# Performance work log

Measured on AMD Instinct MI355X. Metric: run time of the kernel, lower is better.

The kernel has to match this reference:

```python
import jax, jax.numpy as jnp
import numpy as np

B, H, S, D = 2, 16, 8192, 128
NUM_REFLECTIONS = D // 2
ROPE_BASE = 10000.0


def setup_inputs() -> dict:
    key = jax.random.key(0)
    kq, kk, kv = jax.random.split(key, 3)
    q = jax.random.normal(kq, (B, H, S, D), dtype=jnp.float32)
    k = jax.random.normal(kk, (B, H, S, D), dtype=jnp.float32)
    vs = jax.random.normal(kv, (NUM_REFLECTIONS, D), dtype=jnp.float32) * 0.02
    # standard RoPE cos/sin buffer, rotate-half layout: angles duplicated over both halves
    inv_freq = 1.0 / (ROPE_BASE ** (jnp.arange(0, D, 2, dtype=jnp.float32) / D))  # [D/2]
    ang = jnp.arange(S, dtype=jnp.float32)[:, None] * inv_freq[None, :]           # [S, D/2]
    emb = jnp.concatenate([ang, ang], axis=-1)                                    # [S, D]
    cos = jnp.broadcast_to(jnp.cos(emb)[None], (B, S, D))
    sin = jnp.broadcast_to(jnp.sin(emb)[None], (B, S, D))
    return {"q": q, "k": k, "vs": vs, "cos": cos, "sin": sin}


def _householder_matrix(vs):
    # Q = prod of Householder reflections applied left-to-right, as in get_matrix()
    eye = jnp.eye(vs.shape[-1], dtype=vs.dtype)
    def step(Q, v):
        v_norm_sq = jnp.sum(v * v) + 1e-8
        Q = Q - (2.0 / v_norm_sq) * jnp.outer(v, v @ Q)
        return Q, None
    Q, _ = jax.lax.scan(step, eye, vs)
    return Q


def _rotate_half(x):
    d2 = x.shape[-1] // 2
    return jnp.concatenate([-x[..., d2:], x[..., :d2]], axis=-1)


def reference(q, k, vs, cos, sin):
    Q = _householder_matrix(vs)                 # [D, D]
    # inverse transform: x @ Q.T
    qi = jnp.einsum("bhsd,ed->bhse", q, Q)
    ki = jnp.einsum("bhsd,ed->bhse", k, Q)
    c = cos[:, None, :, :]                      # [B,1,S,D] broadcast over heads
    s = sin[:, None, :, :]
    q_rot = qi * c + _rotate_half(qi) * s
    k_rot = ki * c + _rotate_half(ki) * s
    # forward transform: x @ Q
    q_final = jnp.einsum("bhsd,de->bhse", q_rot, Q)
    k_final = jnp.einsum("bhsd,de->bhse", k_rot, Q)
    return (q_final, k_final)
```

## Files before the change

### kernel.cpp

```cpp
#include <hip/hip_runtime.h>

typedef __bf16 bf16x8 __attribute__((ext_vector_type(8)));
typedef __bf16 bf16x4 __attribute__((ext_vector_type(4)));
typedef __bf16 bf16x2 __attribute__((ext_vector_type(2)));
typedef float  f32x4  __attribute__((ext_vector_type(4)));
typedef int    i32x4  __attribute__((ext_vector_type(4)));

static constexpr int kS = 8192;
static constexpr int kD = 128;
static constexpr int kRowsPerTensor = 2 * 16 * kS;
static constexpr int kFragElems = kD * kD;

__global__ __launch_bounds__(1024) void rnrope_build_q(
    const float* __restrict__ vs,
    __bf16* __restrict__ wsQA,
    __bf16* __restrict__ wsQf) {
  __shared__ float vsh[64 * 128];
  const int tid = threadIdx.x;
  for (int i = tid; i < 2048; i += 1024)
    ((float4*)vsh)[i] = ((const float4*)vs)[i];
  __syncthreads();

  const int col  = blockIdx.x * 16 + (tid >> 6);
  const int lane = tid & 63;

  float qlo = (col == lane)      ? 1.0f : 0.0f;
  float qhi = (col == lane + 64) ? 1.0f : 0.0f;

  for (int r = 0; r < 64; ++r) {
    float vlo = vsh[r * 128 + lane];
    float vhi = vsh[r * 128 + lane + 64];
    float t0 = vlo * qlo + vhi * qhi;
    float t1 = vlo * vlo + vhi * vhi;
    #pragma unroll
    for (int off = 32; off > 0; off >>= 1) {
      t0 += __shfl_xor(t0, off);
      t1 += __shfl_xor(t1, off);
    }
    float sf = 2.0f / (t1 + 1e-8f) * t0;
    qlo -= sf * vlo;
    qhi -= sf * vhi;
  }

  {
    const int ks = col >> 5, qdc = (col >> 3) & 3, jj = col & 7;
    #pragma unroll
    for (int h = 0; h < 2; ++h) {
      int i = lane + h * 64;
      float val = h ? qhi : qlo;
      int mt = i >> 4, rl = i & 15;
      wsQA[((mt * 4 + ks) * 64 + qdc * 16 + rl) * 8 + jj] = (__bf16)val;
    }
  }
  {
    const int nt = col >> 4;
    const int nn = col & 15;
    #pragma unroll
    for (int h = 0; h < 2; ++h) {
      int i = lane + h * 64;
      float val = h ? qhi : qlo;
      int ks = i >> 5, qdc = (i >> 3) & 3, jj = i & 7;
      wsQf[((ks * 8 + nt) * 64 + qdc * 16 + nn) * 8 + jj] = (__bf16)val;
    }
  }
}

__global__ __launch_bounds__(512, 4) void rnrope_main(
    const float* __restrict__ qg, const float* __restrict__ kg,
    const __bf16* __restrict__ wsQA, const __bf16* __restrict__ wsQf,
    float* __restrict__ outg) {
  __shared__ __align__(16) __bf16 lds[2 * kFragElems];
  __bf16* ldsQ = lds;
  __bf16* ldsX = lds + kFragElems;

  const int tid    = threadIdx.x;
  const int blk    = blockIdx.x;
  const int tensor = blk >> 11;
  const int tile   = blk & 2047;
  const float* __restrict__ Xg = tensor ? kg : qg;
  float* __restrict__ Og = outg + (size_t)tensor * (size_t)kRowsPerTensor * kD;
  const int row0 = tile * 128;

  #pragma unroll
  for (int i = 0; i < 4; ++i)
    ((uint4*)ldsQ)[tid + i * 512] = ((const uint4*)wsQA)[tid + i * 512];

  #pragma unroll
  for (int it = 0; it < 8; ++it) {
    int f    = tid + it * 512;
    int mloc = f >> 5;
    int q4   = f & 31;
    int k0   = q4 * 4;
    float4 x4 = ((const float4*)(Xg + (size_t)(row0 + mloc) * kD))[q4];
    int ks = k0 >> 5, qdc = (k0 >> 3) & 3, j = k0 & 7;
    int w = mloc >> 4, m = mloc & 15;
    int idx = ((w * 4 + ks) * 64 + qdc * 16 + m) * 8 + j;
    bf16x4 v;
    v[0] = (__bf16)x4.x; v[1] = (__bf16)x4.y; v[2] = (__bf16)x4.z; v[3] = (__bf16)x4.w;
    *(bf16x4*)(&ldsX[idx]) = v;
  }
  __syncthreads();

  const int w    = tid >> 6;
  const int lane = tid & 63;
  const int qd   = lane >> 4;
  const int cc   = lane & 15;

  bf16x8 xb[4];
  #pragma unroll
  for (int ks = 0; ks < 4; ++ks)
    xb[ks] = *(const bf16x8*)(&ldsX[((w * 4 + ks) * 64 + lane) * 8]);

  f32x4 acc[8];
  #pragma unroll
  for (int mt = 0; mt < 8; ++mt) acc[mt] = (f32x4){0.f, 0.f, 0.f, 0.f};
  #pragma unroll
  for (int mt = 0; mt < 8; ++mt) {
    #pragma unroll
    for (int ks = 0; ks < 4; ++ks) {
      bf16x8 a1 = *(const bf16x8*)(&ldsQ[((mt * 4 + ks) * 64 + lane) * 8]);
      acc[mt] = __builtin_amdgcn_mfma_f32_16x16x32_bf16(a1, xb[ks], acc[mt], 0, 0, 0);
    }
  }

  const float kNegL = -0.20762050593046967f;
  {
    float spos = (float)((row0 + w * 16 + cc) & (kS - 1));
    #pragma unroll
    for (int mt = 0; mt < 4; ++mt) {
      #pragma unroll
      for (int reg = 0; reg < 4; ++reg) {
        float fe  = (float)(mt * 16 + qd * 4 + reg);
        float ang = spos * exp2f(kNegL * fe);
        float sv, cv;
        __sincosf(ang, &sv, &cv);
        float ylo = acc[mt][reg];
        float yhi = acc[mt + 4][reg];
        acc[mt][reg]     = ylo * cv - yhi * sv;
        acc[mt + 4][reg] = yhi * cv + ylo * sv;
      }
    }
  }

  int pw[16];
  #pragma unroll
  for (int mt = 0; mt < 8; ++mt) {
    #pragma unroll
    for (int p = 0; p < 2; ++p) {
      bf16x2 t;
      t[0] = (__bf16)acc[mt][2 * p];
      t[1] = (__bf16)acc[mt][2 * p + 1];
      pw[mt * 2 + p] = __builtin_bit_cast(int, t);
    }
  }
  bf16x8 a2[4];
  #pragma unroll
  for (int ks = 0; ks < 4; ++ks) {
    i32x4 aw;
    #pragma unroll
    for (int jw = 0; jw < 4; ++jw) {
      int srcl = ((((2 * qd + (jw >> 1)) & 3) * 16) + cc) * 4;
      int wlo = __builtin_amdgcn_ds_bpermute(srcl, pw[4 * ks + (jw & 1)]);
      int whi = __builtin_amdgcn_ds_bpermute(srcl, pw[4 * ks + 2 + (jw & 1)]);
      aw[jw] = (qd < 2) ? wlo : whi;
    }
    a2[ks] = __builtin_bit_cast(bf16x8, aw);
  }

  #pragma unroll
  for (int nt = 0; nt < 8; ++nt) acc[nt] = (f32x4){0.f, 0.f, 0.f, 0.f};
  #pragma unroll
  for (int nt = 0; nt < 8; ++nt) {
    #pragma unroll
    for (int ks = 0; ks < 4; ++ks) {
      bf16x8 b2 = *(const bf16x8*)(wsQf + ((ks * 8 + nt) * 64 + lane) * 8);
      acc[nt] = __builtin_amdgcn_mfma_f32_16x16x32_bf16(a2[ks], b2, acc[nt], 0, 0, 0);
    }
  }

  float* __restrict__ Ob = Og + (size_t)(row0 + w * 16) * kD;
  #pragma unroll
  for (int nt = 0; nt < 8; ++nt) {
    #pragma unroll
    for (int reg = 0; reg < 4; ++reg)
      Ob[(qd * 4 + reg) * kD + nt * 16 + cc] = acc[nt][reg];
  }
}

extern "C" void kernel_launch(void* const* d_in, const int* in_sizes, int n_in,
                              void* d_out, int out_size, void* d_ws, size_t ws_size,
                              hipStream_t stream) {
  const float* q  = (const float*)d_in[0];
  const float* k  = (const float*)d_in[1];
  const float* vs = (const float*)d_in[2];
  __bf16* wsQA = (__bf16*)d_ws;
  __bf16* wsQf = wsQA + kFragElems;

  rnrope_build_q<<<8, 1024, 0, stream>>>(vs, wsQA, wsQf);
  rnrope_main<<<4096, 512, 0, stream>>>(q, k, wsQA, wsQf, (float*)d_out);
}
```

Baseline: 492.6 us.

## Make main kernel persistent over 64-row tiles with register prefetch of next tile

```diff
diff --git a/kernel.cpp b/kernel.cpp
--- a/kernel.cpp
+++ b/kernel.cpp
@@ -10,6 +10,9 @@
 static constexpr int kD = 128;
 static constexpr int kRowsPerTensor = 2 * 16 * kS;
 static constexpr int kFragElems = kD * kD;
+static constexpr int kTileRows = 64;
+static constexpr int kTilesPerBlock = 8;
+static constexpr int kTilesPerTensor = kRowsPerTensor / kTileRows;
 
 __global__ __launch_bounds__(1024) void rnrope_build_q(
     const float* __restrict__ vs,
@@ -65,125 +68,159 @@
   }
 }
 
-__global__ __launch_bounds__(512, 4) void rnrope_main(
+__device__ __forceinline__ void lds_barrier() {
+  asm volatile("s_waitcnt lgkmcnt(0)" ::: "memory");
+  __builtin_amdgcn_s_barrier();
+  asm volatile("" ::: "memory");
+}
+
+__global__ __launch_bounds__(256, 3) void rnrope_main(
     const float* __restrict__ qg, const float* __restrict__ kg,
     const __bf16* __restrict__ wsQA, const __bf16* __restrict__ wsQf,
     float* __restrict__ outg) {
-  __shared__ __align__(16) __bf16 lds[2 * kFragElems];
-  __bf16* ldsQ = lds;
-  __bf16* ldsX = lds + kFragElems;
-
-  const int tid    = threadIdx.x;
-  const int blk    = blockIdx.x;
-  const int tensor = blk >> 11;
-  const int tile   = blk & 2047;
-  const float* __restrict__ Xg = tensor ? kg : qg;
-  float* __restrict__ Og = outg + (size_t)tensor * (size_t)kRowsPerTensor * kD;
-  const int row0 = tile * 128;
-
-  #pragma unroll
-  for (int i = 0; i < 4; ++i)
-    ((uint4*)ldsQ)[tid + i * 512] = ((const uint4*)wsQA)[tid + i * 512];
-
-  #pragma unroll
-  for (int it = 0; it < 8; ++it) {
-    int f    = tid + it * 512;
-    int mloc = f >> 5;
-    int q4   = f & 31;
-    int k0   = q4 * 4;
-    float4 x4 = ((const float4*)(Xg + (size_t)(row0 + mloc) * kD))[q4];
-    int ks = k0 >> 5, qdc = (k0 >> 3) & 3, j = k0 & 7;
-    int w = mloc >> 4, m = mloc & 15;
-    int idx = ((w * 4 + ks) * 64 + qdc * 16 + m) * 8 + j;
-    bf16x4 v;
-    v[0] = (__bf16)x4.x; v[1] = (__bf16)x4.y; v[2] = (__bf16)x4.z; v[3] = (__bf16)x4.w;
-    *(bf16x4*)(&ldsX[idx]) = v;
-  }
-  __syncthreads();
-
+  __shared__ __align__(16) __bf16 ldsQ[kFragElems];
+  __shared__ __align__(16) __bf16 ldsX[kFragElems / 2];
+
+  const int tid  = threadIdx.x;
   const int w    = tid >> 6;
   const int lane = tid & 63;
   const int qd   = lane >> 4;
   const int cc   = lane & 15;
 
-  bf16x8 xb[4];
   #pragma unroll
-  for (int ks = 0; ks < 4; ++ks)
-    xb[ks] = *(const bf16x8*)(&ldsX[((w * 4 + ks) * 64 + lane) * 8]);
-
-  f32x4 acc[8];
-  #pragma unroll
-  for (int mt = 0; mt < 8; ++mt) acc[mt] = (f32x4){0.f, 0.f, 0.f, 0.f};
-  #pragma unroll
-  for (int mt = 0; mt < 8; ++mt) {
+  for (int i = 0; i < 8; ++i)
+    ((uint4*)ldsQ)[tid + i * 256] = ((const uint4*)wsQA)[tid + i * 256];
+
+  const int g0 = blockIdx.x * kTilesPerBlock;
+
+  float4 xr[8];
+  {
+    const float* __restrict__ Xg = (g0 >> 12) ? kg : qg;
+    const int row0 = (g0 & (kTilesPerTensor - 1)) * kTileRows;
+    #pragma unroll
+    for (int it = 0; it < 8; ++it) {
+      int f = tid + it * 256;
+      int mloc = f >> 5, q4 = f & 31;
+      xr[it] = ((const float4*)(Xg + (size_t)(row0 + mloc) * kD))[q4];
+    }
+  }
+
+  for (int tt = 0; tt < kTilesPerBlock; ++tt) {
+    const int g      = g0 + tt;
+    const int tensor = g >> 12;
+    const int row0   = (g & (kTilesPerTensor - 1)) * kTileRows;
+    float* __restrict__ Og =
+        outg + (size_t)tensor * (size_t)kRowsPerTensor * kD + (size_t)row0 * kD;
+
+    lds_barrier();
+
+    #pragma unroll
+    for (int it = 0; it < 8; ++it) {
+      int f = tid + it * 256;
+      int mloc = f >> 5, q4 = f & 31;
+      int k0 = q4 * 4;
+      int ks = k0 >> 5, qdc = (k0 >> 3) & 3, j = k0 & 7;
+      int ww = mloc >> 4, m = mloc & 15;
+      int idx = ((ww * 4 + ks) * 64 + qdc * 16 + m) * 8 + j;
+      float4 x4 = xr[it];
+      bf16x4 v;
+      v[0] = (__bf16)x4.x; v[1] = (__bf16)x4.y; v[2] = (__bf16)x4.z; v[3] = (__bf16)x4.w;
+      *(bf16x4*)(&ldsX[idx]) = v;
+    }
+
+    if (tt + 1 < kTilesPerBlock) {
+      const int g2 = g + 1;
+      const float* __restrict__ Xg2 = (g2 >> 12) ? kg : qg;
+      const int row02 = (g2 & (kTilesPerTensor - 1)) * kTileRows;
+      #pragma unroll
+      for (int it = 0; it < 8; ++it) {
+        int f = tid + it * 256;
+        int mloc = f >> 5, q4 = f & 31;
+        xr[it] = ((const float4*)(Xg2 + (size_t)(row02 + mloc) * kD))[q4];
+      }
+    }
+
+    lds_barrier();
+
+    bf16x8 xb[4];
+    #pragma unroll
+    for (int ks = 0; ks < 4; ++ks)
+      xb[ks] = *(const bf16x8*)(&ldsX[((w * 4 + ks) * 64 + lane) * 8]);
+
+    f32x4 acc[8];
+    #pragma unroll
+    for (int mt = 0; mt < 8; ++mt) acc[mt] = (f32x4){0.f, 0.f, 0.f, 0.f};
+    #pragma unroll
+    for (int mt = 0; mt < 8; ++mt) {
+      #pragma unroll
+      for (int ks = 0; ks < 4; ++ks) {
+        bf16x8 a1 = *(const bf16x8*)(&ldsQ[((mt * 4 + ks) * 64 + lane) * 8]);
+        acc[mt] = __builtin_amdgcn_mfma_f32_16x16x32_bf16(a1, xb[ks], acc[mt], 0, 0, 0);
+      }
+    }
+
+    const float kNegL = -0.20762050593046967f;
+    {
+      float spos = (float)((row0 + w * 16 + cc) & (kS - 1));
+      #pragma unroll
+      for (int mt = 0; mt < 4; ++mt) {
+        #pragma unroll
+        for (int reg = 0; reg < 4; ++reg) {
+          float fe  = (float)(mt * 16 + qd * 4 + reg);
+          float ang = spos * exp2f(kNegL * fe);
+          float sv, cv;
+          __sincosf(ang, &sv, &cv);
+          float ylo = acc[mt][reg];
+          float yhi = acc[mt + 4][reg];
+          acc[mt][reg]     = ylo * cv - yhi * sv;
+          acc[mt + 4][reg] = yhi * cv + ylo * sv;
+        }
+      }
+    }
+
+    int pw[16];
+    #pragma unroll
+    for (int mt = 0; mt < 8; ++mt) {
+      #pragma unroll
+      for (int p = 0; p < 2; ++p) {
+        bf16x2 t;
+        t[0] = (__bf16)acc[mt][2 * p];
+        t[1] = (__bf16)acc[mt][2 * p + 1];
+        pw[mt * 2 + p] = __builtin_bit_cast(int, t);
+      }
+    }
+    bf16x8 a2[4];
     #pragma unroll
     for (int ks = 0; ks < 4; ++ks) {
-      bf16x8 a1 = *(const bf16x8*)(&ldsQ[((mt * 4 + ks) * 64 + lane) * 8]);
-      acc[mt] = __builtin_amdgcn_mfma_f32_16x16x32_bf16(a1, xb[ks], acc[mt], 0, 0, 0);
-    }
-  }
-
-  const float kNegL = -0.20762050593046967f;
-  {
-    float spos = (float)((row0 + w * 16 + cc) & (kS - 1));
-    #pragma unroll
-    for (int mt = 0; mt < 4; ++mt) {
-      #pragma unroll
-      for (int reg = 0; reg < 4; ++reg) {
-        float fe  = (float)(mt * 16 + qd * 4 + reg);
-        float ang = spos * exp2f(kNegL * fe);
-        float sv, cv;
-        __sincosf(ang, &sv, &cv);
-        float ylo = acc[mt][reg];
-        float yhi = acc[mt + 4][reg];
-        acc[mt][reg]     = ylo * cv - yhi * sv;
-        acc[mt + 4][reg] = yhi * cv + ylo * sv;
-      }
-    }
-  }
-
-  int pw[16];
-  #pragma unroll
-  for (int mt = 0; mt < 8; ++mt) {
-    #pragma unroll
-    for (int p = 0; p < 2; ++p) {
-      bf16x2 t;
-      t[0] = (__bf16)acc[mt][2 * p];
-      t[1] = (__bf16)acc[mt][2 * p + 1];
-      pw[mt * 2 + p] = __builtin_bit_cast(int, t);
-    }
-  }
-  bf16x8 a2[4];
-  #pragma unroll
-  for (int ks = 0; ks < 4; ++ks) {
-    i32x4 aw;
-    #pragma unroll
-    for (int jw = 0; jw < 4; ++jw) {
-      int srcl = ((((2 * qd + (jw >> 1)) & 3) * 16) + cc) * 4;
-      int wlo = __builtin_amdgcn_ds_bpermute(srcl, pw[4 * ks + (jw & 1)]);
-      int whi = __builtin_amdgcn_ds_bpermute(srcl, pw[4 * ks + 2 + (jw & 1)]);
-      aw[jw] = (qd < 2) ? wlo : whi;
-    }
-    a2[ks] = __builtin_bit_cast(bf16x8, aw);
-  }
-
-  #pragma unroll
-  for (int nt = 0; nt < 8; ++nt) acc[nt] = (f32x4){0.f, 0.f, 0.f, 0.f};
-  #pragma unroll
-  for (int nt = 0; nt < 8; ++nt) {
-    #pragma unroll
-    for (int ks = 0; ks < 4; ++ks) {
-      bf16x8 b2 = *(const bf16x8*)(wsQf + ((ks * 8 + nt) * 64 + lane) * 8);
-      acc[nt] = __builtin_amdgcn_mfma_f32_16x16x32_bf16(a2[ks], b2, acc[nt], 0, 0, 0);
-    }
-  }
-
-  float* __restrict__ Ob = Og + (size_t)(row0 + w * 16) * kD;
-  #pragma unroll
-  for (int nt = 0; nt < 8; ++nt) {
-    #pragma unroll
-    for (int reg = 0; reg < 4; ++reg)
-      Ob[(qd * 4 + reg) * kD + nt * 16 + cc] = acc[nt][reg];
+      i32x4 aw;
+      #pragma unroll
+      for (int jw = 0; jw < 4; ++jw) {
+        int srcl = ((((2 * qd + (jw >> 1)) & 3) * 16) + cc) * 4;
+        int wlo = __builtin_amdgcn_ds_bpermute(srcl, pw[4 * ks + (jw & 1)]);
+        int whi = __builtin_amdgcn_ds_bpermute(srcl, pw[4 * ks + 2 + (jw & 1)]);
+        aw[jw] = (qd < 2) ? wlo : whi;
+      }
+      a2[ks] = __builtin_bit_cast(bf16x8, aw);
+    }
+
+    #pragma unroll
+    for (int nt = 0; nt < 8; ++nt) acc[nt] = (f32x4){0.f, 0.f, 0.f, 0.f};
+    #pragma unroll
+    for (int nt = 0; nt < 8; ++nt) {
+      #pragma unroll
+      for (int ks = 0; ks < 4; ++ks) {
+        bf16x8 b2 = *(const bf16x8*)(wsQf + ((ks * 8 + nt) * 64 + lane) * 8);
+        acc[nt] = __builtin_amdgcn_mfma_f32_16x16x32_bf16(a2[ks], b2, acc[nt], 0, 0, 0);
+      }
+    }
+
+    float* __restrict__ Ob = Og + (size_t)(w * 16) * kD;
+    #pragma unroll
+    for (int nt = 0; nt < 8; ++nt) {
+      #pragma unroll
+      for (int reg = 0; reg < 4; ++reg)
+        Ob[(qd * 4 + reg) * kD + nt * 16 + cc] = acc[nt][reg];
+    }
   }
 }
 
@@ -197,5 +234,5 @@
   __bf16* wsQf = wsQA + kFragElems;
 
   rnrope_build_q<<<8, 1024, 0, stream>>>(vs, wsQA, wsQf);
-  rnrope_main<<<4096, 512, 0, stream>>>(q, k, wsQA, wsQf, (float*)d_out);
-}
+  rnrope_main<<<1024, 256, 0, stream>>>(q, k, wsQA, wsQf, (float*)d_out);
+}
```

Result: slower. 635.8 us (+29.1%).
